# Performance work log

Hardware: AMD Instinct MI355X
Metric: run time of the kernel (lower is better)

Reference implementation:

```python
import jax, jax.numpy as jnp
import numpy as np

B, L, D = 2, 1024, 1024
HID, E, K = 2048, 8, 2

def setup_inputs() -> dict:
    key = jax.random.key(0)
    ks = jax.random.split(key, 4)
    std = 0.02
    return {
        "x": jax.random.normal(ks[0], (B, L, D), dtype=jnp.float32),
        "router_scale": jnp.ones((D,), dtype=jnp.float32),
        "router_w": jax.random.normal(ks[1], (D, E), dtype=jnp.float32) * std,
        "gating_w": jax.random.normal(ks[2], (E, 2, HID, D), dtype=jnp.float32) * std,
        "linear_w": jax.random.normal(ks[3], (E, HID, D), dtype=jnp.float32) * std,
        "per_expert_scale": jnp.ones((E,), dtype=jnp.float32),
    }

def reference(x, router_scale, router_w, gating_w, linear_w, per_expert_scale):
    d = x.shape[-1]
    # RMSNorm without scale
    var = jnp.mean(jnp.square(x), axis=-1, keepdims=True)
    r_in = x * jax.lax.rsqrt(var + 1e-6)
    r_in = r_in * jax.lax.rsqrt(jnp.array(d, dtype=r_in.dtype)) * router_scale
    # Router
    logits = jnp.dot(r_in, router_w).astype(jnp.float32)          # [B,L,E]
    probs = jax.nn.softmax(logits, axis=-1)
    _, top_k_idx = jax.lax.top_k(logits, K)                        # [B,L,K]
    indicator = jax.nn.one_hot(top_k_idx, probs.shape[-1], dtype=probs.dtype)  # [B,L,K,E]
    gate_weights = indicator.sum(axis=-2) * probs                  # [B,L,E]
    renorm = jnp.sum(gate_weights, axis=-1, keepdims=True)
    renorm = jnp.where(renorm > 0.0, renorm, 1.0)
    weights = probs / renorm
    top_k_w = jnp.take_along_axis(weights, top_k_idx, axis=-1)     # [B,L,K]
    # Combine weights per expert (indices in top-k are distinct)
    combine = jnp.einsum('blke,blk->ble', indicator, top_k_w)      # [B,L,E]
    combine = combine * per_expert_scale                            # fold per-expert scale
    # Dense all-expert GELU-gated FFN; identical math to per-token gathered weights,
    # since unselected experts get combine weight 0.
    gate0 = jnp.einsum('bld,ehd->bleh', x, gating_w[:, 0])         # [B,L,E,H]
    gate1 = jnp.einsum('bld,ehd->bleh', x, gating_w[:, 1])
    act = jax.nn.gelu(gate0) * gate1                               # approximate gelu, as flax nn.gelu
    out = jnp.einsum('bleh,ehd,ble->bld', act, linear_w, combine)
    return out.astype(x.dtype)
```

## Files before the change

kernel.cpp:

```cpp
#include <hip/hip_runtime.h>
#include <math.h>

#define NB 2
#define NL 1024
#define ND 1024
#define NH 2048
#define NE 8
#define NTOK (NB*NL)
#define NSLOT (NTOK*2)

typedef float f32x4 __attribute__((ext_vector_type(4)));
typedef short s16x8 __attribute__((ext_vector_type(8)));
typedef short s16x4 __attribute__((ext_vector_type(4)));

struct TokMeta { int i0, i1; float w0, w1; };

__device__ __forceinline__ unsigned short f2bf(float f) {
    union { float f; unsigned u; } v; v.f = f;
    unsigned r = v.u + 0x7FFFu + ((v.u >> 16) & 1u);
    return (unsigned short)(r >> 16);
}

__device__ __forceinline__ void gl_lds16(const unsigned short* g, unsigned short* l) {
    __builtin_amdgcn_global_load_lds(
        (const __attribute__((address_space(1))) unsigned int*)(const void*)g,
        (__attribute__((address_space(3))) unsigned int*)(void*)l, 16, 0, 0);
}

__global__ void router_kernel(const float* __restrict__ x,
                              const float* __restrict__ rscale,
                              const float* __restrict__ rw,
                              const float* __restrict__ pes,
                              int* __restrict__ counts,
                              TokMeta* __restrict__ meta)
{
    const int wave = threadIdx.x >> 6;
    const int lane = threadIdx.x & 63;
    const int t = blockIdx.x * 4 + wave;
    const float* xt = x + (size_t)t * ND;

    float part[NE];
#pragma unroll
    for (int e = 0; e < NE; ++e) part[e] = 0.f;
    float ss = 0.f;

#pragma unroll
    for (int i = 0; i < 4; ++i) {
        int d = (lane + 64 * i) * 4;
        float4 xv = *(const float4*)(xt + d);
        float4 sv = *(const float4*)(rscale + d);
        float xs[4] = {xv.x, xv.y, xv.z, xv.w};
        float sc[4] = {sv.x, sv.y, sv.z, sv.w};
        const float* rwp = rw + (size_t)d * NE;
#pragma unroll
        for (int c = 0; c < 4; ++c) {
            float v = xs[c];
            ss += v * v;
            float xr = v * sc[c];
            float4 r0 = *(const float4*)(rwp + c * NE);
            float4 r1 = *(const float4*)(rwp + c * NE + 4);
            part[0] += xr * r0.x; part[1] += xr * r0.y;
            part[2] += xr * r0.z; part[3] += xr * r0.w;
            part[4] += xr * r1.x; part[5] += xr * r1.y;
            part[6] += xr * r1.z; part[7] += xr * r1.w;
        }
    }
#pragma unroll
    for (int off = 32; off > 0; off >>= 1) {
        ss += __shfl_xor(ss, off, 64);
#pragma unroll
        for (int e = 0; e < NE; ++e) part[e] += __shfl_xor(part[e], off, 64);
    }
    if (lane == 0) {
        float rinv = rsqrtf(ss * (1.f / ND) + 1e-6f) * rsqrtf((float)ND);
        float lg[NE];
#pragma unroll
        for (int e = 0; e < NE; ++e) lg[e] = part[e] * rinv;
        int i0 = 0; float b0 = lg[0];
#pragma unroll
        for (int e = 1; e < NE; ++e) if (lg[e] > b0) { b0 = lg[e]; i0 = e; }
        int i1 = -1; float b1 = -INFINITY;
#pragma unroll
        for (int e = 0; e < NE; ++e) if (e != i0 && lg[e] > b1) { b1 = lg[e]; i1 = e; }
        float e1 = expf(b1 - b0);
        float denom = 1.f + e1;
        float w0 = pes[i0] / denom;
        float w1 = pes[i1] * e1 / denom;
        meta[t].i0 = i0; meta[t].i1 = i1; meta[t].w0 = w0; meta[t].w1 = w1;
        atomicAdd(&counts[i0], 1);
        atomicAdd(&counts[i1], 1);
    }
}

__global__ void scan_kernel(const int* __restrict__ counts,
                            int* __restrict__ cursor, int* __restrict__ base)
{
    if (threadIdx.x == 0) {
        int acc = 0;
        for (int e = 0; e < NE; ++e) { base[e] = acc; cursor[e] = acc; acc += counts[e]; }
    }
}

__global__ void scatter_kernel(const TokMeta* __restrict__ meta, int* __restrict__ cursor,
                               int* __restrict__ tok_slot, float* __restrict__ w_slot)
{
    int t = blockIdx.x * blockDim.x + threadIdx.x;
    if (t >= NTOK) return;
    TokMeta m = meta[t];
    int s0 = atomicAdd(&cursor[m.i0], 1);
    tok_slot[s0] = t; w_slot[s0] = m.w0;
    int s1 = atomicAdd(&cursor[m.i1], 1);
    tok_slot[s1] = t; w_slot[s1] = m.w1;
}

__global__ __launch_bounds__(256) void convert_x(const float* __restrict__ x,
                                                 unsigned short* __restrict__ xb)
{
    const size_t i = ((size_t)blockIdx.x * 256 + threadIdx.x) * 8;
    float t[8];
    *(float4*)&t[0] = *(const float4*)(x + i);
    *(float4*)&t[4] = *(const float4*)(x + i + 4);
    s16x8 o;
#pragma unroll
    for (int c = 0; c < 8; ++c) o[c] = (short)f2bf(t[c]);
    *(s16x8*)(xb + i) = o;
}

__global__ __launch_bounds__(256) void convert_gw(const float* __restrict__ gw,
                                                  unsigned short* __restrict__ gwb)
{
    const size_t i = ((size_t)blockIdx.x * 256 + threadIdx.x) * 8;
    float t[8];
    *(float4*)&t[0] = *(const float4*)(gw + i);
    *(float4*)&t[4] = *(const float4*)(gw + i + 4);
    s16x8 o;
#pragma unroll
    for (int c = 0; c < 8; ++c) o[c] = (short)f2bf(t[c]);
    *(s16x8*)(gwb + i) = o;
}

__global__ __launch_bounds__(256) void transpose_lw(const float* __restrict__ lw,
                                                    unsigned short* __restrict__ lwT)
{
    const int e = blockIdx.z;
    const int h0 = blockIdx.y * 64;
    const int d0 = blockIdx.x * 64;
    __shared__ unsigned short T[64][66];

    const int tid = threadIdx.x;
    {
        const int hr = tid >> 2;
        const int dc = (tid & 3) * 16;
        const float* p = lw + ((size_t)e * NH + h0 + hr) * ND + d0 + dc;
        float t[16];
        *(float4*)&t[0]  = *(const float4*)(p);
        *(float4*)&t[4]  = *(const float4*)(p + 4);
        *(float4*)&t[8]  = *(const float4*)(p + 8);
        *(float4*)&t[12] = *(const float4*)(p + 12);
#pragma unroll
        for (int i = 0; i < 8; ++i) {
            unsigned pk = (unsigned)f2bf(t[2 * i]) | ((unsigned)f2bf(t[2 * i + 1]) << 16);
            *(unsigned*)&T[hr][dc + 2 * i] = pk;
        }
    }
    __syncthreads();
    {
        const int dr = tid >> 2;
        const int hc = (tid & 3) * 16;
        s16x8 o0, o1;
#pragma unroll
        for (int i = 0; i < 8; ++i) o0[i] = (short)T[hc + i][dr];
#pragma unroll
        for (int i = 0; i < 8; ++i) o1[i] = (short)T[hc + 8 + i][dr];
        unsigned short* q = lwT + ((size_t)e * ND + d0 + dr) * NH + h0 + hc;
        *(s16x8*)(q)     = o0;
        *(s16x8*)(q + 8) = o1;
    }
}

#define BM 128
#define BH 64
#define BK 32
__global__ __launch_bounds__(256, 2) void gate_gemm(
    const unsigned short* __restrict__ xb, const unsigned short* __restrict__ gwb,
    const int* __restrict__ base, const int* __restrict__ counts,
    const int* __restrict__ tok_slot, const float* __restrict__ w_slot,
    unsigned short* __restrict__ act)
{
    const int e = blockIdx.z;
    const int n = counts[e];
    const int row0 = blockIdx.y * BM;
    if (row0 >= n) return;
    const int b0 = base[e];
    const int h0 = blockIdx.x * BH;

    __shared__ unsigned short As[BM][BK];
    __shared__ unsigned short Bs[BM][BK];
    __shared__ int toks[BM];
    __shared__ float swv[BM];

    const int tid = threadIdx.x;
    if (tid < BM) {
        int r = row0 + tid;
        toks[tid] = (r < n) ? tok_slot[b0 + r] : 0;
        swv[tid]  = (r < n) ? w_slot[b0 + r] : 0.f;
    }
    __syncthreads();

    const int lane = tid & 63;
    const int wid  = tid >> 6;
    const int wm = wid & 1;
    const int wn = wid >> 1;

    const int drow = lane >> 2;
    const int c8  = (((lane & 3) - ((lane >> 3) & 3)) & 3) * 8;
    const int ar0 = wid * 32 + drow;
    const unsigned short* asrc0 = xb + (size_t)toks[ar0] * ND + c8;
    const unsigned short* asrc1 = xb + (size_t)toks[ar0 + 16] * ND + c8;
    const int br0 = wid * 32 + drow;
    const int br1 = br0 + 16;
    const unsigned short* bsrc0 = gwb + (((size_t)e * 2 + (br0 >> 6)) * NH + h0 + (br0 & 63)) * ND + c8;
    const unsigned short* bsrc1 = gwb + (((size_t)e * 2 + (br1 >> 6)) * NH + h0 + (br1 & 63)) * ND + c8;

    f32x4 acc[2][4][2];
#pragma unroll
    for (int gg = 0; gg < 2; ++gg)
#pragma unroll
        for (int i = 0; i < 4; ++i)
#pragma unroll
            for (int j = 0; j < 2; ++j)
                acc[gg][i][j] = (f32x4){0.f, 0.f, 0.f, 0.f};

    const int fr = lane & 15;
    const int pS = (((lane >> 4) + (fr >> 1)) & 3) * 8;

    for (int k0 = 0; k0 < ND; k0 += BK) {
        gl_lds16(asrc0 + k0, &As[wid * 32][0]);
        gl_lds16(asrc1 + k0, &As[wid * 32 + 16][0]);
        gl_lds16(bsrc0 + k0, &Bs[wid * 32][0]);
        gl_lds16(bsrc1 + k0, &Bs[wid * 32 + 16][0]);
        __syncthreads();

        s16x8 af[4], bfr[2][2];
#pragma unroll
        for (int i = 0; i < 4; ++i)
            af[i] = *(const s16x8*)&As[wm * 64 + i * 16 + fr][pS];
#pragma unroll
        for (int gg = 0; gg < 2; ++gg)
#pragma unroll
            for (int j = 0; j < 2; ++j)
                bfr[gg][j] = *(const s16x8*)&Bs[gg * 64 + wn * 32 + j * 16 + fr][pS];
#pragma unroll
        for (int gg = 0; gg < 2; ++gg)
#pragma unroll
            for (int i = 0; i < 4; ++i)
#pragma unroll
                for (int j = 0; j < 2; ++j)
                    acc[gg][i][j] = __builtin_amdgcn_mfma_f32_16x16x32_bf16(
                        af[i], bfr[gg][j], acc[gg][i][j], 0, 0, 0);
        __syncthreads();
    }

    const int rb = (lane >> 4) * 4;
#pragma unroll
    for (int i = 0; i < 4; ++i)
#pragma unroll
        for (int r = 0; r < 4; ++r) {
            int ml = wm * 64 + i * 16 + rb + r;
            int rr = row0 + ml;
            if (rr < n) {
                float w = swv[ml];
#pragma unroll
                for (int j = 0; j < 2; ++j) {
                    float g0v = acc[0][i][j][r];
                    float g1v = acc[1][i][j][r];
                    float u = 0.7978845608028654f * (g0v + 0.044715f * g0v * g0v * g0v);
                    float ex = __expf(2.f * u);
                    float th = 1.f - 2.f / (ex + 1.f);
                    float a = 0.5f * g0v * (1.f + th) * g1v * w;
                    act[(size_t)(b0 + rr) * NH + (h0 + wn * 32 + j * 16 + fr)] = f2bf(a);
                }
            }
        }
}

#define DBM 128
#define DBN 128
#define DBK 32
#define KSPLIT 2
#define KC (NH / KSPLIT)
__global__ __launch_bounds__(256, 2) void down_gemm(
    const unsigned short* __restrict__ act, const unsigned short* __restrict__ lwT,
    const int* __restrict__ base, const int* __restrict__ counts,
    const int* __restrict__ tok_slot, float* __restrict__ out)
{
    const int e  = blockIdx.z >> 1;
    const int kc = blockIdx.z & 1;
    const int n = counts[e];
    const int row0 = blockIdx.y * DBM;
    if (row0 >= n) return;
    const int b0 = base[e];
    const int d0 = blockIdx.x * DBN;

    __shared__ unsigned short As[DBM][DBK];
    __shared__ unsigned short Bs[DBN][DBK];
    __shared__ int stok[DBM];

    const int tid = threadIdx.x;
    if (tid < DBM) {
        int r = row0 + tid;
        stok[tid] = (r < n) ? tok_slot[b0 + r] : 0;
    }
    __syncthreads();

    const int lane = tid & 63;
    const int wid  = tid >> 6;
    const int wm = wid & 1;
    const int wn = wid >> 1;

    const int drow = lane >> 2;
    const int c8  = (((lane & 3) - ((lane >> 3) & 3)) & 3) * 8;
    const int ar0 = wid * 32 + drow;
    const int rr0 = row0 + ar0, rr1 = rr0 + 16;
    const int sl0 = b0 + (rr0 < n ? rr0 : 0);
    const int sl1 = b0 + (rr1 < n ? rr1 : 0);
    const unsigned short* asrc0 = act + (size_t)sl0 * NH + kc * KC + c8;
    const unsigned short* asrc1 = act + (size_t)sl1 * NH + kc * KC + c8;
    const unsigned short* bsrc0 = lwT + ((size_t)e * ND + d0 + ar0) * NH + kc * KC + c8;
    const unsigned short* bsrc1 = bsrc0 + 16 * NH;

    f32x4 acc[4][4];
#pragma unroll
    for (int i = 0; i < 4; ++i)
#pragma unroll
        for (int j = 0; j < 4; ++j)
            acc[i][j] = (f32x4){0.f, 0.f, 0.f, 0.f};

    const int fr = lane & 15;
    const int pS = (((lane >> 4) + (fr >> 1)) & 3) * 8;

    for (int k0 = 0; k0 < KC; k0 += DBK) {
        gl_lds16(asrc0 + k0, &As[wid * 32][0]);
        gl_lds16(asrc1 + k0, &As[wid * 32 + 16][0]);
        gl_lds16(bsrc0 + k0, &Bs[wid * 32][0]);
        gl_lds16(bsrc1 + k0, &Bs[wid * 32 + 16][0]);
        __syncthreads();

        s16x8 af[4], bfr[4];
#pragma unroll
        for (int i = 0; i < 4; ++i)
            af[i] = *(const s16x8*)&As[wm * 64 + i * 16 + fr][pS];
#pragma unroll
        for (int j = 0; j < 4; ++j)
            bfr[j] = *(const s16x8*)&Bs[wn * 64 + j * 16 + fr][pS];
#pragma unroll
        for (int i = 0; i < 4; ++i)
#pragma unroll
            for (int j = 0; j < 4; ++j)
                acc[i][j] = __builtin_amdgcn_mfma_f32_16x16x32_bf16(af[i], bfr[j], acc[i][j], 0, 0, 0);
        __syncthreads();
    }

    const int rb = (lane >> 4) * 4;
#pragma unroll
    for (int i = 0; i < 4; ++i)
#pragma unroll
        for (int r = 0; r < 4; ++r) {
            int ml = wm * 64 + i * 16 + rb + r;
            int rr = row0 + ml;
            if (rr < n) {
                int tok = stok[ml];
#pragma unroll
                for (int j = 0; j < 4; ++j)
                    atomicAdd(&out[(size_t)tok * ND + d0 + wn * 64 + j * 16 + fr],
                              acc[i][j][r]);
            }
        }
}

extern "C" void kernel_launch(void* const* d_in, const int* in_sizes, int n_in,
                              void* d_out, int out_size, void* d_ws, size_t ws_size,
                              hipStream_t stream)
{
    const float* x      = (const float*)d_in[0];
    const float* rscale = (const float*)d_in[1];
    const float* rw     = (const float*)d_in[2];
    const float* gw     = (const float*)d_in[3];
    const float* lw     = (const float*)d_in[4];
    const float* pes    = (const float*)d_in[5];
    float* out = (float*)d_out;

    char* ws = (char*)d_ws;
    int* counts = (int*)ws;
    int* cursor = counts + 8;
    int* base   = counts + 16;
    TokMeta* meta        = (TokMeta*)(ws + 128);
    int*   tok_slot      = (int*)(ws + 33024);
    float* w_slot        = (float*)(ws + 49408);
    unsigned short* xb   = (unsigned short*)(ws + 65792);
    unsigned short* act  = (unsigned short*)(ws + 4260096);
    unsigned short* lwT  = (unsigned short*)(ws + 21037312);
    unsigned short* gwb  = (unsigned short*)(ws + 54591744);

    hipMemsetAsync(d_ws, 0, 128, stream);
    hipMemsetAsync(d_out, 0, (size_t)out_size * sizeof(float), stream);

    router_kernel<<<NTOK / 4, 256, 0, stream>>>(x, rscale, rw, pes, counts, meta);
    scan_kernel<<<1, 64, 0, stream>>>(counts, cursor, base);
    scatter_kernel<<<NTOK / 256, 256, 0, stream>>>(meta, cursor, tok_slot, w_slot);

    convert_x<<<(NTOK * ND) / (256 * 8), 256, 0, stream>>>(x, xb);
    convert_gw<<<(NE * 2 * NH * ND) / (256 * 8), 256, 0, stream>>>(gw, gwb);
    dim3 gt(ND / 64, NH / 64, NE);
    transpose_lw<<<gt, 256, 0, stream>>>(lw, lwT);

    dim3 g2(NH / BH, NTOK / BM, NE);
    gate_gemm<<<g2, 256, 0, stream>>>(xb, gwb, base, counts, tok_slot, w_slot, act);

    dim3 g3(ND / DBN, NTOK / DBM, NE * KSPLIT);
    down_gemm<<<g3, 256, 0, stream>>>(act, lwT, base, counts, tok_slot, out);
}
```

Measured before the change: 455.7 us.

## Fuse routing scatter and x conversion into router, merge weight prep kernels

Measured after the change: 433.7 us. -4.8%, faster.

```diff
diff --git a/kernel.cpp b/kernel.cpp
--- a/kernel.cpp
+++ b/kernel.cpp
@@ -13,8 +13,6 @@
 typedef short s16x8 __attribute__((ext_vector_type(8)));
 typedef short s16x4 __attribute__((ext_vector_type(4)));
 
-struct TokMeta { int i0, i1; float w0, w1; };
-
 __device__ __forceinline__ unsigned short f2bf(float f) {
     union { float f; unsigned u; } v; v.f = f;
     unsigned r = v.u + 0x7FFFu + ((v.u >> 16) & 1u);
@@ -31,13 +29,16 @@
                               const float* __restrict__ rscale,
                               const float* __restrict__ rw,
                               const float* __restrict__ pes,
-                              int* __restrict__ counts,
-                              TokMeta* __restrict__ meta)
+                              int* __restrict__ cursor,
+                              int* __restrict__ tok_slot,
+                              float* __restrict__ w_slot,
+                              unsigned short* __restrict__ xb)
 {
     const int wave = threadIdx.x >> 6;
     const int lane = threadIdx.x & 63;
     const int t = blockIdx.x * 4 + wave;
     const float* xt = x + (size_t)t * ND;
+    unsigned short* xbt = xb + (size_t)t * ND;
 
     float part[NE];
 #pragma unroll
@@ -49,6 +50,10 @@
         int d = (lane + 64 * i) * 4;
         float4 xv = *(const float4*)(xt + d);
         float4 sv = *(const float4*)(rscale + d);
+        s16x4 o;
+        o[0] = (short)f2bf(xv.x); o[1] = (short)f2bf(xv.y);
+        o[2] = (short)f2bf(xv.z); o[3] = (short)f2bf(xv.w);
+        *(s16x4*)(xbt + d) = o;
         float xs[4] = {xv.x, xv.y, xv.z, xv.w};
         float sc[4] = {sv.x, sv.y, sv.z, sv.w};
         const float* rwp = rw + (size_t)d * NE;
@@ -86,68 +91,38 @@
         float denom = 1.f + e1;
         float w0 = pes[i0] / denom;
         float w1 = pes[i1] * e1 / denom;
-        meta[t].i0 = i0; meta[t].i1 = i1; meta[t].w0 = w0; meta[t].w1 = w1;
-        atomicAdd(&counts[i0], 1);
-        atomicAdd(&counts[i1], 1);
-    }
-}
-
-__global__ void scan_kernel(const int* __restrict__ counts,
-                            int* __restrict__ cursor, int* __restrict__ base)
-{
-    if (threadIdx.x == 0) {
-        int acc = 0;
-        for (int e = 0; e < NE; ++e) { base[e] = acc; cursor[e] = acc; acc += counts[e]; }
-    }
-}
-
-__global__ void scatter_kernel(const TokMeta* __restrict__ meta, int* __restrict__ cursor,
-                               int* __restrict__ tok_slot, float* __restrict__ w_slot)
-{
-    int t = blockIdx.x * blockDim.x + threadIdx.x;
-    if (t >= NTOK) return;
-    TokMeta m = meta[t];
-    int s0 = atomicAdd(&cursor[m.i0], 1);
-    tok_slot[s0] = t; w_slot[s0] = m.w0;
-    int s1 = atomicAdd(&cursor[m.i1], 1);
-    tok_slot[s1] = t; w_slot[s1] = m.w1;
-}
-
-__global__ __launch_bounds__(256) void convert_x(const float* __restrict__ x,
-                                                 unsigned short* __restrict__ xb)
-{
-    const size_t i = ((size_t)blockIdx.x * 256 + threadIdx.x) * 8;
-    float t[8];
-    *(float4*)&t[0] = *(const float4*)(x + i);
-    *(float4*)&t[4] = *(const float4*)(x + i + 4);
-    s16x8 o;
-#pragma unroll
-    for (int c = 0; c < 8; ++c) o[c] = (short)f2bf(t[c]);
-    *(s16x8*)(xb + i) = o;
-}
-
-__global__ __launch_bounds__(256) void convert_gw(const float* __restrict__ gw,
-                                                  unsigned short* __restrict__ gwb)
-{
-    const size_t i = ((size_t)blockIdx.x * 256 + threadIdx.x) * 8;
-    float t[8];
-    *(float4*)&t[0] = *(const float4*)(gw + i);
-    *(float4*)&t[4] = *(const float4*)(gw + i + 4);
-    s16x8 o;
-#pragma unroll
-    for (int c = 0; c < 8; ++c) o[c] = (short)f2bf(t[c]);
-    *(s16x8*)(gwb + i) = o;
-}
-
-__global__ __launch_bounds__(256) void transpose_lw(const float* __restrict__ lw,
+        int s0 = atomicAdd(&cursor[i0], 1);
+        tok_slot[i0 * NTOK + s0] = t; w_slot[i0 * NTOK + s0] = w0;
+        int s1 = atomicAdd(&cursor[i1], 1);
+        tok_slot[i1 * NTOK + s1] = t; w_slot[i1 * NTOK + s1] = w1;
+    }
+}
+
+#define GW_BLOCKS ((NE*2*NH*ND) / 2048)
+#define TL_BLOCKS ((ND/64)*(NH/64)*NE)
+__global__ __launch_bounds__(256) void prep_weights(const float* __restrict__ gw,
+                                                    unsigned short* __restrict__ gwb,
+                                                    const float* __restrict__ lw,
                                                     unsigned short* __restrict__ lwT)
 {
-    const int e = blockIdx.z;
-    const int h0 = blockIdx.y * 64;
-    const int d0 = blockIdx.x * 64;
+    const int bid = blockIdx.x;
+    const int tid = threadIdx.x;
+    if (bid < GW_BLOCKS) {
+        const size_t i = ((size_t)bid * 256 + tid) * 8;
+        float t[8];
+        *(float4*)&t[0] = *(const float4*)(gw + i);
+        *(float4*)&t[4] = *(const float4*)(gw + i + 4);
+        s16x8 o;
+#pragma unroll
+        for (int c = 0; c < 8; ++c) o[c] = (short)f2bf(t[c]);
+        *(s16x8*)(gwb + i) = o;
+        return;
+    }
+    const int b2 = bid - GW_BLOCKS;
+    const int d0 = (b2 & 15) * 64;
+    const int h0 = ((b2 >> 4) & 31) * 64;
+    const int e  = b2 >> 9;
     __shared__ unsigned short T[64][66];
-
-    const int tid = threadIdx.x;
     {
         const int hr = tid >> 2;
         const int dc = (tid & 3) * 16;
@@ -181,17 +156,17 @@
 #define BM 128
 #define BH 64
 #define BK 32
-__global__ __launch_bounds__(256, 2) void gate_gemm(
+__global__ __launch_bounds__(256, 3) void gate_gemm(
     const unsigned short* __restrict__ xb, const unsigned short* __restrict__ gwb,
-    const int* __restrict__ base, const int* __restrict__ counts,
+    const int* __restrict__ cursor,
     const int* __restrict__ tok_slot, const float* __restrict__ w_slot,
     unsigned short* __restrict__ act)
 {
     const int e = blockIdx.z;
-    const int n = counts[e];
+    const int n = cursor[e];
     const int row0 = blockIdx.y * BM;
     if (row0 >= n) return;
-    const int b0 = base[e];
+    const int b0 = e * NTOK;
     const int h0 = blockIdx.x * BH;
 
     __shared__ unsigned short As[BM][BK];
@@ -289,17 +264,17 @@
 #define DBK 32
 #define KSPLIT 2
 #define KC (NH / KSPLIT)
-__global__ __launch_bounds__(256, 2) void down_gemm(
+__global__ __launch_bounds__(256, 3) void down_gemm(
     const unsigned short* __restrict__ act, const unsigned short* __restrict__ lwT,
-    const int* __restrict__ base, const int* __restrict__ counts,
+    const int* __restrict__ cursor,
     const int* __restrict__ tok_slot, float* __restrict__ out)
 {
     const int e  = blockIdx.z >> 1;
     const int kc = blockIdx.z & 1;
-    const int n = counts[e];
+    const int n = cursor[e];
     const int row0 = blockIdx.y * DBM;
     if (row0 >= n) return;
-    const int b0 = base[e];
+    const int b0 = e * NTOK;
     const int d0 = blockIdx.x * DBN;
 
     __shared__ unsigned short As[DBM][DBK];
@@ -391,32 +366,25 @@
     float* out = (float*)d_out;
 
     char* ws = (char*)d_ws;
-    int* counts = (int*)ws;
-    int* cursor = counts + 8;
-    int* base   = counts + 16;
-    TokMeta* meta        = (TokMeta*)(ws + 128);
-    int*   tok_slot      = (int*)(ws + 33024);
-    float* w_slot        = (float*)(ws + 49408);
-    unsigned short* xb   = (unsigned short*)(ws + 65792);
-    unsigned short* act  = (unsigned short*)(ws + 4260096);
-    unsigned short* lwT  = (unsigned short*)(ws + 21037312);
-    unsigned short* gwb  = (unsigned short*)(ws + 54591744);
+    int* cursor = (int*)ws;
+    int*   tok_slot      = (int*)(ws + 128);
+    float* w_slot        = (float*)(ws + 65664);
+    unsigned short* xb   = (unsigned short*)(ws + 131200);
+    unsigned short* act  = (unsigned short*)(ws + 4325504);
+    unsigned short* lwT  = (unsigned short*)(ws + 71434368);
+    unsigned short* gwb  = (unsigned short*)(ws + 104988800);
 
     hipMemsetAsync(d_ws, 0, 128, stream);
     hipMemsetAsync(d_out, 0, (size_t)out_size * sizeof(float), stream);
 
-    router_kernel<<<NTOK / 4, 256, 0, stream>>>(x, rscale, rw, pes, counts, meta);
-    scan_kernel<<<1, 64, 0, stream>>>(counts, cursor, base);
-    scatter_kernel<<<NTOK / 256, 256, 0, stream>>>(meta, cursor, tok_slot, w_slot);
-
-    convert_x<<<(NTOK * ND) / (256 * 8), 256, 0, stream>>>(x, xb);
-    convert_gw<<<(NE * 2 * NH * ND) / (256 * 8), 256, 0, stream>>>(gw, gwb);
-    dim3 gt(ND / 64, NH / 64, NE);
-    transpose_lw<<<gt, 256, 0, stream>>>(lw, lwT);
+    router_kernel<<<NTOK / 4, 256, 0, stream>>>(x, rscale, rw, pes, cursor,
+                                                tok_slot, w_slot, xb);
+
+    prep_weights<<<GW_BLOCKS + TL_BLOCKS, 256, 0, stream>>>(gw, gwb, lw, lwT);
 
     dim3 g2(NH / BH, NTOK / BM, NE);
-    gate_gemm<<<g2, 256, 0, stream>>>(xb, gwb, base, counts, tok_slot, w_slot, act);
+    gate_gemm<<<g2, 256, 0, stream>>>(xb, gwb, cursor, tok_slot, w_slot, act);
 
     dim3 g3(ND / DBN, NTOK / DBM, NE * KSPLIT);
-    down_gemm<<<g3, 256, 0, stream>>>(act, lwT, base, counts, tok_slot, out);
-}
+    down_gemm<<<g3, 256, 0, stream>>>(act, lwT, cursor, tok_slot, out);
+}
```
